# Kernel optimization log

Measured on AMD Instinct MI355X. Metric: run time of the kernel, lower is better.

The kernel has to match this reference:

```python
import jax, jax.numpy as jnp
import numpy as np

N_NODES = 100000
N_EDGES = 1600000
IN_DIM = 75
H_COMP = 64
H_BOND = 16
DEPTH = 3


def setup_inputs() -> dict:
    key = jax.random.key(0)
    ks = jax.random.split(key, 8)
    x = jax.random.normal(ks[0], (N_NODES, IN_DIM), dtype=jnp.float32)
    edge_index = jax.random.randint(ks[1], (2, N_EDGES), 0, N_NODES, dtype=jnp.int64)
    edge_attr = jax.random.normal(ks[2], (N_EDGES, H_BOND), dtype=jnp.float32)
    proj_w = jax.random.normal(ks[3], (IN_DIM, H_COMP), dtype=jnp.float32) * (1.0 / np.sqrt(IN_DIM))
    proj_b = jnp.zeros((H_COMP,), dtype=jnp.float32)
    u2_w = jax.random.normal(ks[4], (DEPTH, H_COMP + H_BOND, H_COMP), dtype=jnp.float32) * (1.0 / np.sqrt(H_COMP + H_BOND))
    u2_b = jnp.zeros((DEPTH, H_COMP), dtype=jnp.float32)
    u1_w = jax.random.normal(ks[5], (DEPTH, 2 * H_COMP, H_COMP), dtype=jnp.float32) * (1.0 / np.sqrt(2 * H_COMP))
    u1_b = jnp.zeros((DEPTH, H_COMP), dtype=jnp.float32)
    return {"x": x, "edge_index": edge_index, "edge_attr": edge_attr,
            "proj_w": proj_w, "proj_b": proj_b,
            "u2_w": u2_w, "u2_b": u2_b, "u1_w": u1_w, "u1_b": u1_b}


def reference(x, edge_index, edge_attr, proj_w, proj_b, u2_w, u2_b, u1_w, u1_b):
    # PyG default flow source_to_target: messages gathered from edge_index[0],
    # scatter-added at edge_index[1].
    src, dst = edge_index[0], edge_index[1]
    n = x.shape[0]
    # input projection: [N, in_dim] -> [N, H]
    h = x @ proj_w + proj_b
    for l in range(u2_w.shape[0]):
        # message: concat(x_j, edge_attr) -> Linear -> LeakyReLU(0.1)   [E, H+B] -> [E, H]
        z = jnp.concatenate([h[src], edge_attr], axis=-1)
        m = jax.nn.leaky_relu(z @ u2_w[l] + u2_b[l], negative_slope=0.1)
        # aggregate: scatter-add over destination nodes  [E, H] -> [N, H]
        agg = jax.ops.segment_sum(m, dst, num_segments=n)
        # update: concat(x, agg) -> Linear  [N, 2H] -> [N, H]
        h = jnp.concatenate([h, agg], axis=-1) @ u1_w[l] + u1_b[l]
    return h
```

## Files before the change

kernel.cpp:

```cpp
#include <hip/hip_runtime.h>

typedef __attribute__((ext_vector_type(8))) short frag_ab;
typedef __attribute__((ext_vector_type(4))) float frag_cd;

__device__ __forceinline__ short f2bf(float f) {
  union { float f; unsigned u; } v; v.f = f;
  unsigned r = v.u + 0x7fffu + ((v.u >> 16) & 1u);
  return (short)(r >> 16);
}

__global__ void wconv(const float* __restrict__ W, short* __restrict__ out,
                      int Keff, int S, int nmat)
{
  int tid = blockIdx.x * 256 + threadIdx.x;
  int per = S * 4 * 64;
  if (tid >= nmat * per) return;
  int m = tid / per, r = tid % per;
  int s = r / 256, ct = (r >> 6) & 3, ln = r & 63;
  const float* Wm = W + (size_t)m * Keff * 64;
  __align__(16) short tmp[8];
  for (int j = 0; j < 8; ++j) {
    int k = s * 32 + (ln >> 4) * 8 + j;
    int n = ct * 16 + (ln & 15);
    tmp[j] = (k < Keff) ? f2bf(Wm[k * 64 + n]) : (short)0;
  }
  *(uint4*)&out[((size_t)m * per + (size_t)(s * 4 + ct) * 64 + ln) * 8] = *(uint4*)tmp;
}

#define AS1 104
__global__ __launch_bounds__(256, 4) void proj_kernel(
    const float* __restrict__ x, const short* __restrict__ wt,
    const float* __restrict__ bias, short* __restrict__ hbf, int N)
{
  __shared__ __align__(16) short A[128 * AS1];
  int t = threadIdx.x;
  int nb = blockIdx.x * 128;
  int ln = t & 63;
  frag_ab bf[12];
  for (int s = 0; s < 3; ++s)
    for (int ct = 0; ct < 4; ++ct)
      bf[s * 4 + ct] = *(const frag_ab*)&wt[((size_t)(s * 4 + ct) * 64 + ln) * 8];
  for (int i = 0; i < 48; ++i) {
    int q = i * 256 + t; int el = q / 96; int c = q - el * 96;
    int rg = nb + el;
    float v = (c < 75 && rg < N) ? x[rg * 75 + c] : 0.f;
    A[el * AS1 + c] = f2bf(v);
  }
  __syncthreads();
  int wv = t >> 6;
  int lrow = ln & 15, lk = ln >> 4;
  frag_cd acc[2][4];
  for (int rt = 0; rt < 2; ++rt) for (int ct = 0; ct < 4; ++ct) {
    frag_cd z = {0.f, 0.f, 0.f, 0.f}; acc[rt][ct] = z;
  }
  for (int s = 0; s < 3; ++s) {
    frag_ab a0 = *(const frag_ab*)&A[(wv*32 + lrow) * AS1 + s*32 + lk*8];
    frag_ab a1 = *(const frag_ab*)&A[(wv*32 + 16 + lrow) * AS1 + s*32 + lk*8];
    for (int ct = 0; ct < 4; ++ct) {
      acc[0][ct] = __builtin_amdgcn_mfma_f32_16x16x32_bf16(a0, bf[s*4+ct], acc[0][ct], 0, 0, 0);
      acc[1][ct] = __builtin_amdgcn_mfma_f32_16x16x32_bf16(a1, bf[s*4+ct], acc[1][ct], 0, 0, 0);
    }
  }
  float bv[4];
  for (int ct = 0; ct < 4; ++ct) bv[ct] = bias[ct*16 + lrow];
  for (int rt = 0; rt < 2; ++rt)
    for (int ct = 0; ct < 4; ++ct)
      for (int r = 0; r < 4; ++r) {
        int row = wv*32 + rt*16 + lk*4 + r;
        int rg = nb + row;
        if (rg < N) hbf[(size_t)rg * 64 + ct*16 + lrow] = f2bf(acc[rt][ct][r] + bv[ct]);
      }
}

__global__ __launch_bounds__(256) void hist_kernel(
    const int* __restrict__ dst, int* __restrict__ counts,
    int* __restrict__ rank, int E)
{
  int i = blockIdx.x * 256 + threadIdx.x;
  if (i < E) rank[i] = atomicAdd(&counts[dst[i]], 1);
}

#define SCAN_TILE 2048
__global__ __launch_bounds__(256) void scan_k1(
    const int* __restrict__ counts, int* __restrict__ offsets,
    int* __restrict__ bsum, int n)
{
  __shared__ int ts[256];
  int t = threadIdx.x;
  int base = blockIdx.x * SCAN_TILE + t * 8;
  int v[8]; int s = 0;
  for (int j = 0; j < 8; ++j) { v[j] = (base + j < n) ? counts[base + j] : 0; s += v[j]; }
  ts[t] = s; __syncthreads();
  for (int off = 1; off < 256; off <<= 1) {
    int x = (t >= off) ? ts[t - off] : 0;
    __syncthreads();
    ts[t] += x;
    __syncthreads();
  }
  if (t == 255) bsum[blockIdx.x] = ts[255];
  int run = (t > 0) ? ts[t - 1] : 0;
  for (int j = 0; j < 8; ++j) { if (base + j < n) offsets[base + j] = run; run += v[j]; }
}

__global__ void scan_k2(int* bsum, int nb) {
  int ln = threadIdx.x;
  int v = (ln < nb) ? bsum[ln] : 0;
  int x = v;
  for (int off = 1; off < 64; off <<= 1) {
    int y = __shfl_up(x, off);
    if (ln >= off) x += y;
  }
  if (ln < nb) bsum[ln] = x - v;
}

__global__ __launch_bounds__(256) void scan_k3(
    int* __restrict__ offsets, const int* __restrict__ bsum, int n)
{
  int add = bsum[blockIdx.x];
  int base = blockIdx.x * SCAN_TILE + threadIdx.x;
  for (int j = 0; j < 8; ++j) { int i = base + j * 256; if (i < n) offsets[i] += add; }
}

__global__ __launch_bounds__(256) void scatter_kernel(
    const int* __restrict__ src, const int* __restrict__ dst,
    const float* __restrict__ attr, const int* __restrict__ offsets,
    const int* __restrict__ rank, int2* __restrict__ sd,
    short* __restrict__ attr_s, int E)
{
  int e = blockIdx.x * 256 + threadIdx.x;
  if (e < E) {
    int d = dst[e];
    int p = offsets[d] + rank[e];
    sd[p] = make_int2(src[e], d);
    const float4* a4 = (const float4*)(attr + (size_t)e * 16);
    float4 v0 = a4[0], v1 = a4[1], v2 = a4[2], v3 = a4[3];
    __align__(16) short tmp[16];
    tmp[0]=f2bf(v0.x); tmp[1]=f2bf(v0.y); tmp[2]=f2bf(v0.z); tmp[3]=f2bf(v0.w);
    tmp[4]=f2bf(v1.x); tmp[5]=f2bf(v1.y); tmp[6]=f2bf(v1.z); tmp[7]=f2bf(v1.w);
    tmp[8]=f2bf(v2.x); tmp[9]=f2bf(v2.y); tmp[10]=f2bf(v2.z); tmp[11]=f2bf(v2.w);
    tmp[12]=f2bf(v3.x); tmp[13]=f2bf(v3.y); tmp[14]=f2bf(v3.z); tmp[15]=f2bf(v3.w);
    *(uint4*)&attr_s[(size_t)p * 16]     = *(uint4*)&tmp[0];
    *(uint4*)&attr_s[(size_t)p * 16 + 8] = *(uint4*)&tmp[8];
  }
}

#define MS 66
__global__ __launch_bounds__(256, 4) void msg_kernel(
    const short* __restrict__ hbf, const short* __restrict__ attr_s,
    const int2* __restrict__ sd, const short* __restrict__ wt,
    const float* __restrict__ bias, float* __restrict__ agg, int E)
{
  __shared__ float M[128 * MS];
  __shared__ int dstl[128];
  int t = threadIdx.x;
  int eb = blockIdx.x * 128;
  int ln = t & 63;
  int wv = t >> 6;
  int lrow = ln & 15, lk = ln >> 4;

  if (t < 128) dstl[t] = (eb + t < E) ? sd[eb + t].y : -1;

  int p0 = eb + wv*32 + lrow;  if (p0 > E - 1) p0 = E - 1;
  int p1 = p0 + 16;            if (p1 > E - 1) p1 = E - 1;
  int s0 = sd[p0].x, s1 = sd[p1].x;

  frag_ab a[3][2];
  a[0][0] = *(const frag_ab*)&hbf[(size_t)s0 * 64 + lk*8];
  a[0][1] = *(const frag_ab*)&hbf[(size_t)s1 * 64 + lk*8];
  a[1][0] = *(const frag_ab*)&hbf[(size_t)s0 * 64 + 32 + lk*8];
  a[1][1] = *(const frag_ab*)&hbf[(size_t)s1 * 64 + 32 + lk*8];
  frag_ab z8 = {0,0,0,0,0,0,0,0};
  a[2][0] = (lk < 2) ? *(const frag_ab*)&attr_s[(size_t)p0 * 16 + lk*8] : z8;
  a[2][1] = (lk < 2) ? *(const frag_ab*)&attr_s[(size_t)p1 * 16 + lk*8] : z8;

  frag_cd acc[2][4];
  for (int rt = 0; rt < 2; ++rt) for (int ct = 0; ct < 4; ++ct) {
    frag_cd z = {0.f, 0.f, 0.f, 0.f}; acc[rt][ct] = z;
  }
  for (int s = 0; s < 3; ++s)
    for (int ct = 0; ct < 4; ++ct) {
      frag_ab b = *(const frag_ab*)&wt[((size_t)(s * 4 + ct) * 64 + ln) * 8];
      acc[0][ct] = __builtin_amdgcn_mfma_f32_16x16x32_bf16(a[s][0], b, acc[0][ct], 0, 0, 0);
      acc[1][ct] = __builtin_amdgcn_mfma_f32_16x16x32_bf16(a[s][1], b, acc[1][ct], 0, 0, 0);
    }
  float bv[4];
  for (int ct = 0; ct < 4; ++ct) bv[ct] = bias[ct*16 + lrow];

  for (int rt = 0; rt < 2; ++rt)
    for (int ct = 0; ct < 4; ++ct)
      for (int r = 0; r < 4; ++r) {
        int row = wv*32 + rt*16 + lk*4 + r;
        float m = acc[rt][ct][r] + bv[ct];
        m = m > 0.f ? m : 0.1f * m;
        M[row * MS + ct*16 + lrow] = m;
      }
  __syncthreads();

  {
    int lo = wv * 32;
    bool end = false;
    if (ln < 32) {
      int di = dstl[lo + ln];
      end = (ln == 31) || (di != dstl[lo + ln + 1]);
    }
    unsigned long long bm = __ballot(end);
    unsigned em = (unsigned)bm;
    unsigned cm = em & ~(em & (0u - em)) & 0x7fffffffu;

    float s = 0.f;
#pragma unroll
    for (int i = 0; i < 32; ++i) {
      s += M[(lo + i) * MS + ln];
      if ((em >> i) & 1u) {
        int d = __builtin_amdgcn_readfirstlane(dstl[lo + i]);
        if (d >= 0) {
          float* dest = &agg[(size_t)d * 64 + ln];
          if ((cm >> i) & 1u) *dest = s;
          else unsafeAtomicAdd(dest, s);
        }
        s = 0.f;
      }
    }
  }
}

__global__ __launch_bounds__(256, 4) void upd_kernel(
    const short* __restrict__ hbf, float* __restrict__ agg,
    const short* __restrict__ wt, const float* __restrict__ bias,
    float* __restrict__ hout, short* __restrict__ hbfo, int N, int last)
{
  int t = threadIdx.x;
  int nb = blockIdx.x * 128;
  int ln = t & 63;
  int wv = t >> 6;
  int lrow = ln & 15, lk = ln >> 4;
  int r0 = nb + wv*32 + lrow;
  int r1 = r0 + 16;

  frag_ab z8 = {0,0,0,0,0,0,0,0};
  frag_ab a[4][2];
  a[0][0] = (r0 < N) ? *(const frag_ab*)&hbf[(size_t)r0 * 64 + lk*8]      : z8;
  a[0][1] = (r1 < N) ? *(const frag_ab*)&hbf[(size_t)r1 * 64 + lk*8]      : z8;
  a[1][0] = (r0 < N) ? *(const frag_ab*)&hbf[(size_t)r0 * 64 + 32 + lk*8] : z8;
  a[1][1] = (r1 < N) ? *(const frag_ab*)&hbf[(size_t)r1 * 64 + 32 + lk*8] : z8;
  for (int si = 0; si < 2; ++si) {
    int cb = si * 32 + lk * 8;
    for (int rt = 0; rt < 2; ++rt) {
      int rg = rt ? r1 : r0;
      frag_ab af = z8;
      if (rg < N) {
        float* ap = &agg[(size_t)rg * 64 + cb];
        float4 v0 = *(const float4*)ap;
        float4 v1 = *(const float4*)(ap + 4);
        af[0]=f2bf(v0.x); af[1]=f2bf(v0.y); af[2]=f2bf(v0.z); af[3]=f2bf(v0.w);
        af[4]=f2bf(v1.x); af[5]=f2bf(v1.y); af[6]=f2bf(v1.z); af[7]=f2bf(v1.w);
        if (!last) {
          float4 z = make_float4(0.f, 0.f, 0.f, 0.f);
          *(float4*)ap = z; *(float4*)(ap + 4) = z;
        }
      }
      a[2 + si][rt] = af;
    }
  }

  frag_cd acc[2][4];
  for (int rt = 0; rt < 2; ++rt) for (int ct = 0; ct < 4; ++ct) {
    frag_cd z = {0.f, 0.f, 0.f, 0.f}; acc[rt][ct] = z;
  }
  for (int s = 0; s < 4; ++s)
    for (int ct = 0; ct < 4; ++ct) {
      frag_ab b = *(const frag_ab*)&wt[((size_t)(s * 4 + ct) * 64 + ln) * 8];
      acc[0][ct] = __builtin_amdgcn_mfma_f32_16x16x32_bf16(a[s][0], b, acc[0][ct], 0, 0, 0);
      acc[1][ct] = __builtin_amdgcn_mfma_f32_16x16x32_bf16(a[s][1], b, acc[1][ct], 0, 0, 0);
    }
  float bv[4];
  for (int ct = 0; ct < 4; ++ct) bv[ct] = bias[ct*16 + lrow];
  for (int rt = 0; rt < 2; ++rt)
    for (int ct = 0; ct < 4; ++ct)
      for (int r = 0; r < 4; ++r) {
        int row = wv*32 + rt*16 + lk*4 + r;
        int rg = nb + row;
        if (rg < N) {
          float v = acc[rt][ct][r] + bv[ct];
          if (last) hout[(size_t)rg * 64 + ct*16 + lrow] = v;
          hbfo[(size_t)rg * 64 + ct*16 + lrow] = f2bf(v);
        }
      }
}

extern "C" void kernel_launch(void* const* d_in, const int* in_sizes, int n_in,
                              void* d_out, int out_size, void* d_ws, size_t ws_size,
                              hipStream_t stream) {
  const float* x    = (const float*)d_in[0];
  const int*   ei   = (const int*)d_in[1];
  const float* attr = (const float*)d_in[2];
  const float* pw   = (const float*)d_in[3];
  const float* pb   = (const float*)d_in[4];
  const float* u2w  = (const float*)d_in[5];
  const float* u2b  = (const float*)d_in[6];
  const float* u1w  = (const float*)d_in[7];
  const float* u1b  = (const float*)d_in[8];

  const int N = in_sizes[0] / 75;
  const int E = in_sizes[1] / 2;
  const int* src = ei;
  const int* dst = ei + E;

  float* hout = (float*)d_out;
  char*  ws   = (char*)d_ws;
  size_t nh   = (size_t)N * 64;
  size_t off  = 0;
  short* hbf   = (short*)(ws + off); off += nh * 2;
  float* agg   = (float*)(ws + off); off += nh * 4;
  int2*  sd    = (int2*) (ws + off); off += (size_t)E * 8;
  short* attr_s= (short*)(ws + off); off += (size_t)E * 32;
  int*   rank  = (int*)  (ws + off); off += (size_t)E * 4;
  short* projt = (short*)(ws + off); off += 3 * 4 * 64 * 8 * 2;
  short* u2t   = (short*)(ws + off); off += (size_t)3 * 3 * 4 * 64 * 8 * 2;
  short* u1t   = (short*)(ws + off); off += (size_t)3 * 4 * 4 * 64 * 8 * 2;
  int* counts  = (int*)agg;
  int* offsets = counts + N;
  int* bsum    = offsets + N;

  const int NB = (N + 127) / 128;
  const int EB = (E + 127) / 128;
  const int GE = (E + 255) / 256;
  const int NS = (N + SCAN_TILE - 1) / SCAN_TILE;

  wconv<<<3, 256, 0, stream>>>(pw, projt, 75, 3, 1);
  wconv<<<9, 256, 0, stream>>>(u2w, u2t, 80, 3, 3);
  wconv<<<12, 256, 0, stream>>>(u1w, u1t, 128, 4, 3);
  proj_kernel<<<NB, 256, 0, stream>>>(x, projt, pb, hbf, N);
  hipMemsetAsync(counts, 0, (size_t)N * 4, stream);
  hist_kernel<<<GE, 256, 0, stream>>>(dst, counts, rank, E);
  scan_k1<<<NS, 256, 0, stream>>>(counts, offsets, bsum, N);
  scan_k2<<<1, 64, 0, stream>>>(bsum, NS);
  scan_k3<<<NS, 256, 0, stream>>>(offsets, bsum, N);
  scatter_kernel<<<GE, 256, 0, stream>>>(src, dst, attr, offsets, rank,
                                         sd, attr_s, E);

  hipMemsetAsync(agg, 0, nh * 4, stream);
  for (int l = 0; l < 3; ++l) {
    msg_kernel<<<EB, 256, 0, stream>>>(hbf, attr_s, sd,
                                       u2t + (size_t)l * 6144, u2b + l * 64,
                                       agg, E);
    upd_kernel<<<NB, 256, 0, stream>>>(hbf, agg,
                                       u1t + (size_t)l * 8192, u1b + l * 64,
                                       hout, hbf, N, l == 2);
  }
}
```

Measured before the change: 695.9 us.

## Pack edge records into one AoS buffer and fuse the small setup kernels

Replaces the separate src/dst pair array and the bf16 edge-attribute array with a single 64-byte per-edge record holding src, dst and attributes. The goal is for the message kernel to fetch all per-edge data from one cache region. The three weight-conversion launches are merged into one kernel, and the single-block scan kernel is folded into the offset-add kernel, which removes launches. The rank buffer now lives in the agg workspace. The padded record raises per-edge bytes from 40 to 64, which may add memory traffic in each layer.

Result: no change. 702.8 us (+1.0%).

```diff
diff --git a/kernel.cpp b/kernel.cpp
--- a/kernel.cpp
+++ b/kernel.cpp
@@ -9,10 +9,10 @@
   return (short)(r >> 16);
 }
 
-__global__ void wconv(const float* __restrict__ W, short* __restrict__ out,
-                      int Keff, int S, int nmat)
-{
-  int tid = blockIdx.x * 256 + threadIdx.x;
+__device__ __forceinline__ void wconv_body(
+    const float* __restrict__ W, short* __restrict__ out,
+    int Keff, int S, int nmat, int tid)
+{
   int per = S * 4 * 64;
   if (tid >= nmat * per) return;
   int m = tid / per, r = tid % per;
@@ -25,6 +25,17 @@
     tmp[j] = (k < Keff) ? f2bf(Wm[k * 64 + n]) : (short)0;
   }
   *(uint4*)&out[((size_t)m * per + (size_t)(s * 4 + ct) * 64 + ln) * 8] = *(uint4*)tmp;
+}
+
+__global__ void wconv_all(const float* __restrict__ pw,
+                          const float* __restrict__ u2w,
+                          const float* __restrict__ u1w,
+                          short* projt, short* u2t, short* u1t)
+{
+  int b = blockIdx.x, t = threadIdx.x;
+  if (b < 3)        wconv_body(pw,  projt, 75,  3, 1, b * 256 + t);
+  else if (b < 12)  wconv_body(u2w, u2t,   80,  3, 3, (b - 3) * 256 + t);
+  else              wconv_body(u1w, u1t,   128, 4, 3, (b - 12) * 256 + t);
 }
 
 #define AS1 104
@@ -102,36 +113,34 @@
   for (int j = 0; j < 8; ++j) { if (base + j < n) offsets[base + j] = run; run += v[j]; }
 }
 
-__global__ void scan_k2(int* bsum, int nb) {
-  int ln = threadIdx.x;
-  int v = (ln < nb) ? bsum[ln] : 0;
-  int x = v;
-  for (int off = 1; off < 64; off <<= 1) {
-    int y = __shfl_up(x, off);
-    if (ln >= off) x += y;
-  }
-  if (ln < nb) bsum[ln] = x - v;
-}
-
 __global__ __launch_bounds__(256) void scan_k3(
-    int* __restrict__ offsets, const int* __restrict__ bsum, int n)
-{
-  int add = bsum[blockIdx.x];
-  int base = blockIdx.x * SCAN_TILE + threadIdx.x;
+    int* __restrict__ offsets, const int* __restrict__ bsum, int n, int nb)
+{
+  __shared__ int adds;
+  int t = threadIdx.x;
+  if (t < 64) {
+    int v = (t < nb) ? bsum[t] : 0;
+    int x = v;
+    for (int o = 1; o < 64; o <<= 1) { int y = __shfl_up(x, o); if (t >= o) x += y; }
+    int b = blockIdx.x;
+    int a = __shfl(x, b - 1);
+    if (t == 0) adds = (b == 0) ? 0 : a;
+  }
+  __syncthreads();
+  int add = adds;
+  int base = blockIdx.x * SCAN_TILE + t;
   for (int j = 0; j < 8; ++j) { int i = base + j * 256; if (i < n) offsets[i] += add; }
 }
 
 __global__ __launch_bounds__(256) void scatter_kernel(
     const int* __restrict__ src, const int* __restrict__ dst,
     const float* __restrict__ attr, const int* __restrict__ offsets,
-    const int* __restrict__ rank, int2* __restrict__ sd,
-    short* __restrict__ attr_s, int E)
+    const int* __restrict__ rank, uint4* __restrict__ rec, int E)
 {
   int e = blockIdx.x * 256 + threadIdx.x;
   if (e < E) {
     int d = dst[e];
     int p = offsets[d] + rank[e];
-    sd[p] = make_int2(src[e], d);
     const float4* a4 = (const float4*)(attr + (size_t)e * 16);
     float4 v0 = a4[0], v1 = a4[1], v2 = a4[2], v3 = a4[3];
     __align__(16) short tmp[16];
@@ -139,16 +148,21 @@
     tmp[4]=f2bf(v1.x); tmp[5]=f2bf(v1.y); tmp[6]=f2bf(v1.z); tmp[7]=f2bf(v1.w);
     tmp[8]=f2bf(v2.x); tmp[9]=f2bf(v2.y); tmp[10]=f2bf(v2.z); tmp[11]=f2bf(v2.w);
     tmp[12]=f2bf(v3.x); tmp[13]=f2bf(v3.y); tmp[14]=f2bf(v3.z); tmp[15]=f2bf(v3.w);
-    *(uint4*)&attr_s[(size_t)p * 16]     = *(uint4*)&tmp[0];
-    *(uint4*)&attr_s[(size_t)p * 16 + 8] = *(uint4*)&tmp[8];
+    uint4* rp = rec + (size_t)p * 4;
+    uint4 q0; q0.x = (unsigned)src[e]; q0.y = (unsigned)d; q0.z = 0u; q0.w = 0u;
+    uint4 qz = {0u, 0u, 0u, 0u};
+    rp[0] = q0;
+    rp[1] = *(uint4*)&tmp[0];
+    rp[2] = *(uint4*)&tmp[8];
+    rp[3] = qz;
   }
 }
 
 #define MS 66
 __global__ __launch_bounds__(256, 4) void msg_kernel(
-    const short* __restrict__ hbf, const short* __restrict__ attr_s,
-    const int2* __restrict__ sd, const short* __restrict__ wt,
-    const float* __restrict__ bias, float* __restrict__ agg, int E)
+    const short* __restrict__ hbf, const uint4* __restrict__ rec,
+    const short* __restrict__ wt, const float* __restrict__ bias,
+    float* __restrict__ agg, int E)
 {
   __shared__ float M[128 * MS];
   __shared__ int dstl[128];
@@ -158,11 +172,15 @@
   int wv = t >> 6;
   int lrow = ln & 15, lk = ln >> 4;
 
-  if (t < 128) dstl[t] = (eb + t < E) ? sd[eb + t].y : -1;
+  if (t < 128) {
+    int p = eb + t;
+    dstl[t] = (p < E) ? ((const int*)(rec + (size_t)p * 4))[1] : -1;
+  }
 
   int p0 = eb + wv*32 + lrow;  if (p0 > E - 1) p0 = E - 1;
   int p1 = p0 + 16;            if (p1 > E - 1) p1 = E - 1;
-  int s0 = sd[p0].x, s1 = sd[p1].x;
+  int s0 = ((const int*)(rec + (size_t)p0 * 4))[0];
+  int s1 = ((const int*)(rec + (size_t)p1 * 4))[0];
 
   frag_ab a[3][2];
   a[0][0] = *(const frag_ab*)&hbf[(size_t)s0 * 64 + lk*8];
@@ -170,8 +188,8 @@
   a[1][0] = *(const frag_ab*)&hbf[(size_t)s0 * 64 + 32 + lk*8];
   a[1][1] = *(const frag_ab*)&hbf[(size_t)s1 * 64 + 32 + lk*8];
   frag_ab z8 = {0,0,0,0,0,0,0,0};
-  a[2][0] = (lk < 2) ? *(const frag_ab*)&attr_s[(size_t)p0 * 16 + lk*8] : z8;
-  a[2][1] = (lk < 2) ? *(const frag_ab*)&attr_s[(size_t)p1 * 16 + lk*8] : z8;
+  a[2][0] = (lk < 2) ? *(const frag_ab*)((const short*)(rec + (size_t)p0 * 4) + 8 + lk*8) : z8;
+  a[2][1] = (lk < 2) ? *(const frag_ab*)((const short*)(rec + (size_t)p1 * 4) + 8 + lk*8) : z8;
 
   frag_cd acc[2][4];
   for (int rt = 0; rt < 2; ++rt) for (int ct = 0; ct < 4; ++ct) {
@@ -312,36 +330,31 @@
   size_t off  = 0;
   short* hbf   = (short*)(ws + off); off += nh * 2;
   float* agg   = (float*)(ws + off); off += nh * 4;
-  int2*  sd    = (int2*) (ws + off); off += (size_t)E * 8;
-  short* attr_s= (short*)(ws + off); off += (size_t)E * 32;
-  int*   rank  = (int*)  (ws + off); off += (size_t)E * 4;
+  uint4* rec   = (uint4*)(ws + off); off += (size_t)E * 64;
   short* projt = (short*)(ws + off); off += 3 * 4 * 64 * 8 * 2;
   short* u2t   = (short*)(ws + off); off += (size_t)3 * 3 * 4 * 64 * 8 * 2;
   short* u1t   = (short*)(ws + off); off += (size_t)3 * 4 * 4 * 64 * 8 * 2;
   int* counts  = (int*)agg;
   int* offsets = counts + N;
   int* bsum    = offsets + N;
+  int* rank    = bsum + 64;
 
   const int NB = (N + 127) / 128;
   const int EB = (E + 127) / 128;
   const int GE = (E + 255) / 256;
   const int NS = (N + SCAN_TILE - 1) / SCAN_TILE;
 
-  wconv<<<3, 256, 0, stream>>>(pw, projt, 75, 3, 1);
-  wconv<<<9, 256, 0, stream>>>(u2w, u2t, 80, 3, 3);
-  wconv<<<12, 256, 0, stream>>>(u1w, u1t, 128, 4, 3);
+  wconv_all<<<24, 256, 0, stream>>>(pw, u2w, u1w, projt, u2t, u1t);
   proj_kernel<<<NB, 256, 0, stream>>>(x, projt, pb, hbf, N);
   hipMemsetAsync(counts, 0, (size_t)N * 4, stream);
   hist_kernel<<<GE, 256, 0, stream>>>(dst, counts, rank, E);
   scan_k1<<<NS, 256, 0, stream>>>(counts, offsets, bsum, N);
-  scan_k2<<<1, 64, 0, stream>>>(bsum, NS);
-  scan_k3<<<NS, 256, 0, stream>>>(offsets, bsum, N);
-  scatter_kernel<<<GE, 256, 0, stream>>>(src, dst, attr, offsets, rank,
-                                         sd, attr_s, E);
+  scan_k3<<<NS, 256, 0, stream>>>(offsets, bsum, N, NS);
+  scatter_kernel<<<GE, 256, 0, stream>>>(src, dst, attr, offsets, rank, rec, E);
 
   hipMemsetAsync(agg, 0, nh * 4, stream);
   for (int l = 0; l < 3; ++l) {
-    msg_kernel<<<EB, 256, 0, stream>>>(hbf, attr_s, sd,
+    msg_kernel<<<EB, 256, 0, stream>>>(hbf, rec,
                                        u2t + (size_t)l * 6144, u2b + l * 64,
                                        agg, E);
     upd_kernel<<<NB, 256, 0, stream>>>(hbf, agg,
```
